# Performance work log

Hardware: AMD Instinct MI355X
Metric: run time of the kernel (lower is better)

## Reference

```python
import jax, jax.numpy as jnp
import numpy as np

B, T, D, H = 512, 128, 384, 6
DH = D // H  # 64
DFF = 4 * D  # 1536
EPS = 1e-5


def layer_norm(x, g, b):
    mu = jnp.mean(x, axis=-1, keepdims=True)
    var = jnp.var(x, axis=-1, keepdims=True)
    return (x - mu) * jax.lax.rsqrt(var + EPS) * g + b


def setup_inputs() -> dict:
    key = jax.random.key(0)
    ks = jax.random.split(key, 12)
    s = lambda *sh: 1.0 / np.sqrt(sh[0])
    return {
        "x": jax.random.normal(ks[0], (B, T, D), dtype=jnp.float32),
        "Wq": jax.random.normal(ks[1], (D, D), dtype=jnp.float32) * s(D),
        "Wk": jax.random.normal(ks[2], (D, D), dtype=jnp.float32) * s(D),
        "Wv": jax.random.normal(ks[3], (D, D), dtype=jnp.float32) * s(D),
        "Wo": jax.random.normal(ks[4], (D, D), dtype=jnp.float32) * s(D),
        "bo": jnp.zeros((D,), jnp.float32),
        "W1": jax.random.normal(ks[5], (D, DFF), dtype=jnp.float32) * s(D),
        "b1": jnp.zeros((DFF,), jnp.float32),
        "W2": jax.random.normal(ks[6], (DFF, D), dtype=jnp.float32) * s(DFF),
        "b2": jnp.zeros((D,), jnp.float32),
        "g1": jnp.ones((D,), jnp.float32),
        "be1": jnp.zeros((D,), jnp.float32),
        "g2": jnp.ones((D,), jnp.float32),
        "be2": jnp.zeros((D,), jnp.float32),
    }


def reference(x, Wq, Wk, Wv, Wo, bo, W1, b1, W2, b2, g1, be1, g2, be2):
    # --- multi-head causal self-attention on layer_norm1(x) ---
    h = layer_norm(x, g1, be1)
    q = (h @ Wq).reshape(B, T, H, DH)
    k = (h @ Wk).reshape(B, T, H, DH)
    v = (h @ Wv).reshape(B, T, H, DH)
    scores = jnp.einsum("bthd,bshd->bhts", q, k) * (DH ** -0.5)  # [B,H,T,T]
    causal = jnp.tril(jnp.ones((T, T), dtype=bool))
    scores = jnp.where(causal, scores, -jnp.inf)
    attn = jax.nn.softmax(scores, axis=-1)
    o = jnp.einsum("bhts,bshd->bthd", attn, v).reshape(B, T, D)
    x = x + o @ Wo + bo
    # --- feed-forward on layer_norm2(x) ---
    h2 = layer_norm(x, g2, be2)
    ff = jax.nn.relu(h2 @ W1 + b1) @ W2 + b2
    return x + ff
```

## Files before the change

### kernel.cpp

```cpp
#include <hip/hip_runtime.h>

#define B_   512
#define T_   128
#define D_   384
#define H_   6
#define DH_  64
#define DFF_ 1536
#define NROW (B_*T_)

typedef __attribute__((ext_vector_type(8))) short bf16x8;
typedef __attribute__((ext_vector_type(4))) float f32x4;

__device__ __forceinline__ unsigned short f2bf(float f) {
  union { float f; unsigned u; } v; v.f = f;
  unsigned r = v.u + 0x7fffu + ((v.u >> 16) & 1u);
  return (unsigned short)(r >> 16);
}

#define GLDS16(gp, lp)                                                     \
  __builtin_amdgcn_global_load_lds(                                        \
      (const __attribute__((address_space(1))) void*)(gp),                 \
      (__attribute__((address_space(3))) void*)(lp), 16, 0, 0)

#define BAR_LGKM() asm volatile("s_waitcnt lgkmcnt(0)\n\ts_barrier" ::: "memory")

__global__ void wt_kernel(const float* __restrict__ W, unsigned short* __restrict__ WT,
                          int K, int Nn) {
  int id = blockIdx.x * 256 + threadIdx.x;
  if (id >= K * Nn) return;
  int n = id % Nn, kk = id / Nn;
  WT[(size_t)n * K + kk] = f2bf(W[(size_t)kk * Nn + n]);
}

__global__ void pack_w1(const unsigned short* __restrict__ W1T,
                        unsigned short* __restrict__ W1P) {
  int tid = blockIdx.x * 256 + threadIdx.x;
  int lane = tid & 63, frag = tid >> 6;
  int k = frag % 12, t2 = frag / 12;
  int mi = t2 & 1, t3 = t2 >> 1;
  int w = t3 & 3, c = t3 >> 2;
  int l15 = lane & 15, lq = lane >> 4;
  int r = c * 128 + w * 32 + mi * 16 + l15;
  int col = k * 32 + lq * 8;
  *(int4*)(W1P + (size_t)tid * 8) = *(const int4*)(W1T + (size_t)r * 384 + col);
}
__global__ void pack_w2(const unsigned short* __restrict__ W2T,
                        unsigned short* __restrict__ W2P) {
  int tid = blockIdx.x * 256 + threadIdx.x;
  int lane = tid & 63, frag = tid >> 6;
  int kk = frag & 3, t2 = frag >> 2;
  int c = t2 % 12, t3 = t2 / 12;
  int mi = t3 % 6, w = t3 / 6;
  int l15 = lane & 15, lq = lane >> 4;
  int r = w * 96 + mi * 16 + l15;
  int col = c * 128 + kk * 32 + lq * 8;
  *(int4*)(W2P + (size_t)tid * 8) = *(const int4*)(W2T + (size_t)r * 1536 + col);
}

__global__ __launch_bounds__(256) void ln_kernel(const float* __restrict__ x,
                                                 const float* __restrict__ g,
                                                 const float* __restrict__ be,
                                                 unsigned short* __restrict__ out) {
  int row = (blockIdx.x * 256 + threadIdx.x) >> 6;
  int l = threadIdx.x & 63;
  const float* xr = x + (size_t)row * D_;
  float v[6]; float s = 0.f, ss = 0.f;
  #pragma unroll
  for (int i = 0; i < 6; ++i) { v[i] = xr[l + i*64]; s += v[i]; ss += v[i]*v[i]; }
  #pragma unroll
  for (int m = 1; m < 64; m <<= 1) { s += __shfl_xor(s, m); ss += __shfl_xor(ss, m); }
  float mu  = s * (1.f / D_);
  float var = ss * (1.f / D_) - mu * mu;
  float rs  = rsqrtf(var + 1e-5f);
  unsigned short* orow = out + (size_t)row * D_;
  #pragma unroll
  for (int i = 0; i < 6; ++i) {
    int c = l + i*64;
    orow[c] = f2bf((v[i] - mu) * rs * g[c] + be[c]);
  }
}

template<int EPI>
__global__ __launch_bounds__(256) void gemm_bt(const unsigned short* __restrict__ A,
                                               const unsigned short* __restrict__ BT,
                                               void* __restrict__ Cc,
                                               const float* __restrict__ bias,
                                               const float* __restrict__ res,
                                               int Nn, int K) {
  __shared__ unsigned short As[2][128][32];
  __shared__ unsigned short Bs[2][128][32];
  int tid = threadIdx.x, w = tid >> 6, l = tid & 63;
  int wr = w >> 1, wc = w & 1;
  size_t R0 = (size_t)blockIdx.x * 128;
  int C0 = blockIdx.y * 128;

  int seg0 = (w * 2 + 0) * 16;
  int seg1 = (w * 2 + 1) * 16;
  int srow0 = seg0 + (l >> 2);
  int srow1 = seg1 + (l >> 2);
  int scol  = (l & 3) * 8;

  const unsigned short* ga0 = A  + (R0 + srow0) * K + scol;
  const unsigned short* ga1 = A  + (R0 + srow1) * K + scol;
  const unsigned short* gb0 = BT + (size_t)(C0 + srow0) * K + scol;
  const unsigned short* gb1 = BT + (size_t)(C0 + srow1) * K + scol;

  f32x4 acc[4][4];
  #pragma unroll
  for (int i = 0; i < 4; ++i)
    #pragma unroll
    for (int j = 0; j < 4; ++j) acc[i][j] = (f32x4){0.f, 0.f, 0.f, 0.f};

  GLDS16(ga0, &As[0][seg0][0]);
  GLDS16(ga1, &As[0][seg1][0]);
  GLDS16(gb0, &Bs[0][seg0][0]);
  GLDS16(gb1, &Bs[0][seg1][0]);
  ga0 += 32; ga1 += 32; gb0 += 32; gb1 += 32;

  int nk = K >> 5;
  for (int t = 0; t < nk; ++t) {
    int cur = t & 1;
    __syncthreads();
    if (t + 1 < nk) {
      GLDS16(ga0, &As[cur ^ 1][seg0][0]);
      GLDS16(ga1, &As[cur ^ 1][seg1][0]);
      GLDS16(gb0, &Bs[cur ^ 1][seg0][0]);
      GLDS16(gb1, &Bs[cur ^ 1][seg1][0]);
      ga0 += 32; ga1 += 32; gb0 += 32; gb1 += 32;
    }
    bf16x8 af[4], bf[4];
    #pragma unroll
    for (int mi = 0; mi < 4; ++mi)
      af[mi] = *(const bf16x8*)(&As[cur][wr*64 + mi*16 + (l & 15)][(l >> 4) * 8]);
    #pragma unroll
    for (int ni = 0; ni < 4; ++ni)
      bf[ni] = *(const bf16x8*)(&Bs[cur][wc*64 + ni*16 + (l & 15)][(l >> 4) * 8]);
    #pragma unroll
    for (int mi = 0; mi < 4; ++mi)
      #pragma unroll
      for (int ni = 0; ni < 4; ++ni)
        acc[mi][ni] = __builtin_amdgcn_mfma_f32_16x16x32_bf16(af[mi], bf[ni], acc[mi][ni], 0, 0, 0);
  }

  #pragma unroll
  for (int mi = 0; mi < 4; ++mi) {
    #pragma unroll
    for (int ni = 0; ni < 4; ++ni) {
      int col = C0 + wc*64 + ni*16 + (l & 15);
      #pragma unroll
      for (int j = 0; j < 4; ++j) {
        size_t row = R0 + wr*64 + mi*16 + ((l >> 4) << 2) + j;
        float vv = acc[mi][ni][j];
        if (EPI == 1) {
          ((float*)Cc)[row * Nn + col] = vv + bias[col] + res[row * Nn + col];
        } else {
          int buf = col / 384, c2 = col - buf * 384;
          ((unsigned short*)Cc)[(size_t)buf * NROW * 384 + row * 384 + c2] = f2bf(vv);
        }
      }
    }
  }
}

#define LDA3(dst, pA, k0)                                                    \
  { _Pragma("unroll") for (int kq = 0; kq < 3; ++kq)                         \
      dst[kq] = *(const bf16x8*)((pA) + ((k0) + kq) * 512); }

#define CMP3(buf, k0, acc)                                                   \
  { _Pragma("unroll") for (int kq = 0; kq < 3; ++kq) {                       \
      bf16x8 bfr[4];                                                         \
      _Pragma("unroll") for (int ni = 0; ni < 4; ++ni)                       \
        bfr[ni] = *(const bf16x8*)(smem + (ni*12 + (k0)+kq)*1024 + l*16);    \
      _Pragma("unroll") for (int ni = 0; ni < 4; ++ni)                       \
        acc[ni] = __builtin_amdgcn_mfma_f32_16x16x32_bf16(                   \
            buf[kq], bfr[ni], acc[ni], 0, 0, 0);                             \
    } }

__global__ __launch_bounds__(512, 4) void ffn_fused(
    const unsigned short* __restrict__ h2,
    const unsigned short* __restrict__ w1P,
    const unsigned short* __restrict__ w2P,
    const float* __restrict__ b1,
    const float* __restrict__ b2,
    float* __restrict__ out)
{
  __shared__ __align__(16) char smem[65536];
  int tid = threadIdx.x, w = tid >> 6, l = tid & 63;
  int l15 = l & 15, lq = l >> 4;
  size_t R0 = (size_t)blockIdx.x * 64;

  {
    int row = tid >> 3, gi = row >> 4, l15w = row & 15;
    int cbase = (tid & 7) * 48;
    const unsigned short* src = h2 + (R0 + row) * 384 + cbase;
    #pragma unroll
    for (int i = 0; i < 6; ++i) {
      int col = cbase + i * 8;
      int k = col >> 5, lqw = (col >> 3) & 3;
      *(int4*)(smem + (gi*12 + k)*1024 + (lqw*16 + l15w)*16) = *(const int4*)(src + i*8);
    }
  }
  __syncthreads();

  f32x4 oacc[3][4];
  #pragma unroll
  for (int i = 0; i < 3; ++i)
    #pragma unroll
    for (int j = 0; j < 4; ++j) oacc[i][j] = (f32x4){0.f, 0.f, 0.f, 0.f};

  const unsigned short* w1b = w1P + w * 6144  + l * 8;
  const unsigned short* w2b = w2P + w * 73728 + l * 8;

  #define LDV(dst, pV, kk)                                                   \
    { _Pragma("unroll") for (int mi = 0; mi < 3; ++mi)                       \
        dst[mi] = *(const bf16x8*)((pV) + mi * 24576 + (kk) * 512); }

  #define CMPV(buf, kk)                                                      \
    { bf16x8 bv[4];                                                          \
      _Pragma("unroll") for (int ni = 0; ni < 4; ++ni)                       \
        bv[ni] = *(const bf16x8*)(smem + 49152 + (ni*4 + (kk))*1024 + l*16); \
      _Pragma("unroll") for (int mi = 0; mi < 3; ++mi)                       \
        _Pragma("unroll") for (int ni = 0; ni < 4; ++ni)                     \
          oacc[mi][ni] = __builtin_amdgcn_mfma_f32_16x16x32_bf16(            \
              buf[mi], bv[ni], oacc[mi][ni], 0, 0, 0);                       \
    }

  bf16x8 afA[3], afB[3];
  bf16x8 avA[3], avB[3];

  LDA3(afA, w1b, 0)

  for (int c = 0; c < 12; ++c) {
    const unsigned short* pA = w1b + (size_t)c * 49152;
    const unsigned short* pV = w2b + c * 2048;

    f32x4 pacc[4];
    #pragma unroll
    for (int j = 0; j < 4; ++j) pacc[j] = (f32x4){0.f, 0.f, 0.f, 0.f};

    LDA3(afB, pA, 3)
    __builtin_amdgcn_s_setprio(1); CMP3(afA, 0, pacc) __builtin_amdgcn_s_setprio(0);
    LDA3(afA, pA, 6)
    __builtin_amdgcn_s_setprio(1); CMP3(afB, 3, pacc) __builtin_amdgcn_s_setprio(0);
    LDA3(afB, pA, 9)
    __builtin_amdgcn_s_setprio(1); CMP3(afA, 6, pacc) __builtin_amdgcn_s_setprio(0);
    LDV(avA, pV, 0)
    __builtin_amdgcn_s_setprio(1); CMP3(afB, 9, pacc) __builtin_amdgcn_s_setprio(0);

    {
      int fcb = c * 128 + w * 16 + lq * 4;
      float4 bb = *(const float4*)(b1 + fcb);
      unsigned pw = (unsigned)(49152 + (w >> 1) * 1024 +
                    (((w & 1) * 2 + (lq >> 1)) * 16 + l15) * 16 + (lq & 1) * 8);
      #pragma unroll
      for (int ni = 0; ni < 4; ++ni) {
        float p0 = pacc[ni][0] + bb.x;
        float p1 = pacc[ni][1] + bb.y;
        float p2 = pacc[ni][2] + bb.z;
        float p3 = pacc[ni][3] + bb.w;
        ushort4 pk;
        pk.x = f2bf(p0 > 0.f ? p0 : 0.f);
        pk.y = f2bf(p1 > 0.f ? p1 : 0.f);
        pk.z = f2bf(p2 > 0.f ? p2 : 0.f);
        pk.w = f2bf(p3 > 0.f ? p3 : 0.f);
        *(ushort4*)(smem + pw + ni * 4096) = pk;
      }
    }
    BAR_LGKM();

    const unsigned short* pAn = w1b + (size_t)(c < 11 ? c + 1 : 11) * 49152;
    LDV(avB, pV, 1)
    __builtin_amdgcn_s_setprio(1); CMPV(avA, 0) __builtin_amdgcn_s_setprio(0);
    LDV(avA, pV, 2)
    __builtin_amdgcn_s_setprio(1); CMPV(avB, 1) __builtin_amdgcn_s_setprio(0);
    LDV(avB, pV, 3)
    __builtin_amdgcn_s_setprio(1); CMPV(avA, 2) __builtin_amdgcn_s_setprio(0);
    LDA3(afA, pAn, 0)
    __builtin_amdgcn_s_setprio(1); CMPV(avB, 3) __builtin_amdgcn_s_setprio(0);
    BAR_LGKM();
  }
  #undef LDV
  #undef CMPV

  #pragma unroll
  for (int mi = 0; mi < 3; ++mi) {
    int ocb = w * 48 + mi * 16 + lq * 4;
    float4 b2v = *(const float4*)(b2 + ocb);
    #pragma unroll
    for (int ni = 0; ni < 4; ++ni) {
      size_t row = R0 + ni * 16 + l15;
      float* op = out + row * D_ + ocb;
      float4 r = *(const float4*)op;
      float4 o;
      o.x = oacc[mi][ni][0] + b2v.x + r.x;
      o.y = oacc[mi][ni][1] + b2v.y + r.y;
      o.z = oacc[mi][ni][2] + b2v.z + r.z;
      o.w = oacc[mi][ni][3] + b2v.w + r.w;
      *(float4*)op = o;
    }
  }
}

__global__ __launch_bounds__(256) void attn_kernel(const unsigned short* __restrict__ q,
                                                   const unsigned short* __restrict__ k,
                                                   const unsigned short* __restrict__ v,
                                                   unsigned short* __restrict__ o) {
  __shared__ __align__(16) char smem[52224];
  unsigned short (*Ks)[72]       = (unsigned short(*)[72])smem;
  unsigned short (*Ps)[32][136]  = (unsigned short(*)[32][136])smem;
  unsigned short (*Vt)[136]      = (unsigned short(*)[136])(smem + 34816);

  int bh = blockIdx.x;
  int b = bh / H_, h = bh % H_;
  int tid = threadIdx.x, w = tid >> 6, l = tid & 63;

  const unsigned short* kb = k + ((size_t)b * T_) * D_ + h * DH_;
  const unsigned short* vb = v + ((size_t)b * T_) * D_ + h * DH_;
  #pragma unroll
  for (int it = 0; it < 4; ++it) {
    int id = it * 256 + tid;
    int s = id >> 3, c8 = (id & 7) * 8;
    int4 kv = *(const int4*)(kb + (size_t)s * D_ + c8);
    *(int4*)(&Ks[s][c8]) = kv;
    int4 vv = *(const int4*)(vb + (size_t)s * D_ + c8);
    const unsigned short* pe = (const unsigned short*)&vv;
    #pragma unroll
    for (int j2 = 0; j2 < 8; ++j2) Vt[c8 + j2][s] = pe[j2];
  }
  __syncthreads();

  const unsigned short* qbp = q + ((size_t)b * T_) * D_ + h * DH_;
  int rowbase = w * 32;
  bf16x8 aq[2][2];
  #pragma unroll
  for (int mi = 0; mi < 2; ++mi)
    #pragma unroll
    for (int ks = 0; ks < 2; ++ks)
      aq[mi][ks] = *(const bf16x8*)(qbp + (size_t)(rowbase + mi*16 + (l & 15)) * D_
                                        + ks*32 + ((l >> 4) << 3));

  f32x4 accs[2][8];
  #pragma unroll
  for (int i = 0; i < 2; ++i)
    #pragma unroll
    for (int j = 0; j < 8; ++j) accs[i][j] = (f32x4){0.f, 0.f, 0.f, 0.f};
  #pragma unroll
  for (int ks = 0; ks < 2; ++ks) {
    bf16x8 bk[8];
    #pragma unroll
    for (int ni = 0; ni < 8; ++ni)
      bk[ni] = *(const bf16x8*)(&Ks[ni*16 + (l & 15)][ks*32 + ((l >> 4) << 3)]);
    __builtin_amdgcn_s_setprio(1);
    #pragma unroll
    for (int mi = 0; mi < 2; ++mi)
      #pragma unroll
      for (int ni = 0; ni < 8; ++ni)
        accs[mi][ni] = __builtin_amdgcn_mfma_f32_16x16x32_bf16(aq[mi][ks], bk[ni], accs[mi][ni], 0, 0, 0);
    __builtin_amdgcn_s_setprio(0);
  }
  __syncthreads();

  #pragma unroll
  for (int mi = 0; mi < 2; ++mi) {
    #pragma unroll
    for (int j = 0; j < 4; ++j) {
      int t = rowbase + mi*16 + ((l >> 4) << 2) + j;
      float mx = -1e30f;
      #pragma unroll
      for (int ni = 0; ni < 8; ++ni) {
        int scol = ni*16 + (l & 15);
        float sv = accs[mi][ni][j] * 0.125f;
        sv = (scol <= t) ? sv : -1e30f;
        accs[mi][ni][j] = sv;
        mx = fmaxf(mx, sv);
      }
      mx = fmaxf(mx, __shfl_xor(mx, 1));
      mx = fmaxf(mx, __shfl_xor(mx, 2));
      mx = fmaxf(mx, __shfl_xor(mx, 4));
      mx = fmaxf(mx, __shfl_xor(mx, 8));
      float sum = 0.f;
      #pragma unroll
      for (int ni = 0; ni < 8; ++ni) {
        float e = __expf(accs[mi][ni][j] - mx);
        accs[mi][ni][j] = e;
        sum += e;
      }
      sum += __shfl_xor(sum, 1);
      sum += __shfl_xor(sum, 2);
      sum += __shfl_xor(sum, 4);
      sum += __shfl_xor(sum, 8);
      float inv = 1.f / sum;
      #pragma unroll
      for (int ni = 0; ni < 8; ++ni)
        Ps[w][mi*16 + ((l >> 4) << 2) + j][ni*16 + (l & 15)] = f2bf(accs[mi][ni][j] * inv);
    }
  }
  __syncthreads();

  f32x4 acco[2][4];
  #pragma unroll
  for (int i = 0; i < 2; ++i)
    #pragma unroll
    for (int j = 0; j < 4; ++j) acco[i][j] = (f32x4){0.f, 0.f, 0.f, 0.f};
  #pragma unroll
  for (int ks = 0; ks < 4; ++ks) {
    bf16x8 ap[2], bv[4];
    #pragma unroll
    for (int mi = 0; mi < 2; ++mi)
      ap[mi] = *(const bf16x8*)(&Ps[w][mi*16 + (l & 15)][ks*32 + ((l >> 4) << 3)]);
    #pragma unroll
    for (int ni = 0; ni < 4; ++ni)
      bv[ni] = *(const bf16x8*)(&Vt[ni*16 + (l & 15)][ks*32 + ((l >> 4) << 3)]);
    __builtin_amdgcn_s_setprio(1);
    #pragma unroll
    for (int mi = 0; mi < 2; ++mi)
      #pragma unroll
      for (int ni = 0; ni < 4; ++ni)
        acco[mi][ni] = __builtin_amdgcn_mfma_f32_16x16x32_bf16(ap[mi], bv[ni], acco[mi][ni], 0, 0, 0);
    __builtin_amdgcn_s_setprio(0);
  }

  unsigned short* ob = o + ((size_t)b * T_) * D_ + h * DH_;
  #pragma unroll
  for (int mi = 0; mi < 2; ++mi)
    #pragma unroll
    for (int ni = 0; ni < 4; ++ni)
      #pragma unroll
      for (int j = 0; j < 4; ++j) {
        int t = rowbase + mi*16 + ((l >> 4) << 2) + j;
        int d = ni*16 + (l & 15);
        ob[(size_t)t * D_ + d] = f2bf(acco[mi][ni][j]);
      }
}

extern "C" void kernel_launch(void* const* d_in, const int* in_sizes, int n_in,
                              void* d_out, int out_size, void* d_ws, size_t ws_size,
                              hipStream_t stream) {
  const float* x   = (const float*)d_in[0];
  const float* Wq  = (const float*)d_in[1];
  const float* Wk  = (const float*)d_in[2];
  const float* Wv  = (const float*)d_in[3];
  const float* Wo  = (const float*)d_in[4];
  const float* bo  = (const float*)d_in[5];
  const float* W1  = (const float*)d_in[6];
  const float* b1  = (const float*)d_in[7];
  const float* W2  = (const float*)d_in[8];
  const float* b2  = (const float*)d_in[9];
  const float* g1  = (const float*)d_in[10];
  const float* be1 = (const float*)d_in[11];
  const float* g2  = (const float*)d_in[12];
  const float* be2 = (const float*)d_in[13];

  char* ws = (char*)d_ws;
  unsigned short* hb   = (unsigned short*)(ws);
  unsigned short* qb   = (unsigned short*)(ws +  50331648);
  unsigned short* kbuf = (unsigned short*)(ws + 100663296);
  unsigned short* vbuf = (unsigned short*)(ws + 150994944);
  unsigned short* wqT  = (unsigned short*)(ws + 201326592);
  unsigned short* wkT  = wqT + 147456;
  unsigned short* wvT  = wkT + 147456;
  unsigned short* woT  = wvT + 147456;
  unsigned short* w1T  = woT + 147456;
  unsigned short* w2T  = w1T + 589824;
  unsigned short* w1P  = w2T + 589824;
  unsigned short* w2P  = w1P + 589824;
  float* x2 = (float*)d_out;
  (void)kbuf; (void)vbuf;

  wt_kernel<<<dim3(576),  256, 0, stream>>>(Wq, wqT, 384, 384);
  wt_kernel<<<dim3(576),  256, 0, stream>>>(Wk, wkT, 384, 384);
  wt_kernel<<<dim3(576),  256, 0, stream>>>(Wv, wvT, 384, 384);
  wt_kernel<<<dim3(576),  256, 0, stream>>>(Wo, woT, 384, 384);
  wt_kernel<<<dim3(2304), 256, 0, stream>>>(W1, w1T, 384, 1536);
  wt_kernel<<<dim3(2304), 256, 0, stream>>>(W2, w2T, 1536, 384);
  pack_w1<<<dim3(288), 256, 0, stream>>>(w1T, w1P);
  pack_w2<<<dim3(288), 256, 0, stream>>>(w2T, w2P);

  ln_kernel<<<dim3(NROW / 4), 256, 0, stream>>>(x, g1, be1, hb);

  gemm_bt<3><<<dim3(NROW / 128, 9), 256, 0, stream>>>(hb, wqT, qb, nullptr, nullptr, 1152, 384);

  attn_kernel<<<dim3(B_ * H_), 256, 0, stream>>>(qb, kbuf, vbuf, qb);

  gemm_bt<1><<<dim3(NROW / 128, 3), 256, 0, stream>>>(qb, woT, x2, bo, x, 384, 384);

  ln_kernel<<<dim3(NROW / 4), 256, 0, stream>>>((const float*)x2, g2, be2, hb);

  ffn_fused<<<dim3(NROW / 64), 512, 0, stream>>>(hb, w1P, w2P, b1, b2, x2);
}
```

Measured before the change: 453.3 us.

## Use 32x32x16 MFMA for FFN first GEMM with 256-wide hidden chunks

Restructures the fused FFN kernel so the W1 GEMM uses 32x32x16 bf16 MFMA instructions over 256-column hidden chunks (6 iterations instead of 12), with a new W1 packing layout and h2 LDS layout to match. The second GEMM consumes 8 k-steps per chunk, which halves the number of barriers per row block. The intent is to cut LDS fragment reads and loop overhead per FLOP. In exchange the kernel needs 80KB of dynamic shared memory, which can reduce occupancy, and it drops the register double-buffered prefetch of weights used before.

```diff
diff --git a/kernel.cpp b/kernel.cpp
--- a/kernel.cpp
+++ b/kernel.cpp
@@ -10,6 +10,7 @@
 
 typedef __attribute__((ext_vector_type(8))) short bf16x8;
 typedef __attribute__((ext_vector_type(4))) float f32x4;
+typedef __attribute__((ext_vector_type(16))) float f32x16;
 
 __device__ __forceinline__ unsigned short f2bf(float f) {
   union { float f; unsigned u; } v; v.f = f;
@@ -32,17 +33,15 @@
   WT[(size_t)n * K + kk] = f2bf(W[(size_t)kk * Nn + n]);
 }
 
-__global__ void pack_w1(const unsigned short* __restrict__ W1T,
-                        unsigned short* __restrict__ W1P) {
+__global__ void pack_w1_32(const unsigned short* __restrict__ W1T,
+                           unsigned short* __restrict__ W1P) {
   int tid = blockIdx.x * 256 + threadIdx.x;
   int lane = tid & 63, frag = tid >> 6;
-  int k = frag % 12, t2 = frag / 12;
-  int mi = t2 & 1, t3 = t2 >> 1;
-  int w = t3 & 3, c = t3 >> 2;
-  int l15 = lane & 15, lq = lane >> 4;
-  int r = c * 128 + w * 32 + mi * 16 + l15;
-  int col = k * 32 + lq * 8;
-  *(int4*)(W1P + (size_t)tid * 8) = *(const int4*)(W1T + (size_t)r * 384 + col);
+  int k16 = frag % 24, t = frag / 24;
+  int w = t & 7, c6 = t >> 3;
+  int row = c6 * 256 + w * 32 + (lane & 31);
+  int col = k16 * 16 + (lane >> 5) * 8;
+  *(int4*)(W1P + (size_t)tid * 8) = *(const int4*)(W1T + (size_t)row * 384 + col);
 }
 __global__ void pack_w2(const unsigned short* __restrict__ W2T,
                         unsigned short* __restrict__ W2P) {
@@ -162,20 +161,6 @@
   }
 }
 
-#define LDA3(dst, pA, k0)                                                    \
-  { _Pragma("unroll") for (int kq = 0; kq < 3; ++kq)                         \
-      dst[kq] = *(const bf16x8*)((pA) + ((k0) + kq) * 512); }
-
-#define CMP3(buf, k0, acc)                                                   \
-  { _Pragma("unroll") for (int kq = 0; kq < 3; ++kq) {                       \
-      bf16x8 bfr[4];                                                         \
-      _Pragma("unroll") for (int ni = 0; ni < 4; ++ni)                       \
-        bfr[ni] = *(const bf16x8*)(smem + (ni*12 + (k0)+kq)*1024 + l*16);    \
-      _Pragma("unroll") for (int ni = 0; ni < 4; ++ni)                       \
-        acc[ni] = __builtin_amdgcn_mfma_f32_16x16x32_bf16(                   \
-            buf[kq], bfr[ni], acc[ni], 0, 0, 0);                             \
-    } }
-
 __global__ __launch_bounds__(512, 4) void ffn_fused(
     const unsigned short* __restrict__ h2,
     const unsigned short* __restrict__ w1P,
@@ -184,20 +169,20 @@
     const float* __restrict__ b2,
     float* __restrict__ out)
 {
-  __shared__ __align__(16) char smem[65536];
+  extern __shared__ __align__(16) char smem[];
   int tid = threadIdx.x, w = tid >> 6, l = tid & 63;
   int l15 = l & 15, lq = l >> 4;
   size_t R0 = (size_t)blockIdx.x * 64;
 
   {
-    int row = tid >> 3, gi = row >> 4, l15w = row & 15;
-    int cbase = (tid & 7) * 48;
-    const unsigned short* src = h2 + (R0 + row) * 384 + cbase;
+    int row = tid >> 3, nt = row >> 5, r31 = row & 31;
+    const unsigned short* src = h2 + (R0 + row) * 384;
     #pragma unroll
     for (int i = 0; i < 6; ++i) {
-      int col = cbase + i * 8;
-      int k = col >> 5, lqw = (col >> 3) & 3;
-      *(int4*)(smem + (gi*12 + k)*1024 + (lqw*16 + l15w)*16) = *(const int4*)(src + i*8);
+      int c8 = (tid & 7) + i * 8;
+      int k16 = c8 >> 1, hi = c8 & 1;
+      *(int4*)(smem + (nt*24 + k16)*1024 + (hi*32 + r31)*16) =
+          *(const int4*)(src + c8 * 8);
     }
   }
   __syncthreads();
@@ -208,79 +193,79 @@
     #pragma unroll
     for (int j = 0; j < 4; ++j) oacc[i][j] = (f32x4){0.f, 0.f, 0.f, 0.f};
 
-  const unsigned short* w1b = w1P + w * 6144  + l * 8;
+  const unsigned short* w1b = w1P + w * 12288 + l * 8;
   const unsigned short* w2b = w2P + w * 73728 + l * 8;
 
-  #define LDV(dst, pV, kk)                                                   \
-    { _Pragma("unroll") for (int mi = 0; mi < 3; ++mi)                       \
-        dst[mi] = *(const bf16x8*)((pV) + mi * 24576 + (kk) * 512); }
-
-  #define CMPV(buf, kk)                                                      \
-    { bf16x8 bv[4];                                                          \
-      _Pragma("unroll") for (int ni = 0; ni < 4; ++ni)                       \
-        bv[ni] = *(const bf16x8*)(smem + 49152 + (ni*4 + (kk))*1024 + l*16); \
-      _Pragma("unroll") for (int mi = 0; mi < 3; ++mi)                       \
-        _Pragma("unroll") for (int ni = 0; ni < 4; ++ni)                     \
-          oacc[mi][ni] = __builtin_amdgcn_mfma_f32_16x16x32_bf16(            \
-              buf[mi], bv[ni], oacc[mi][ni], 0, 0, 0);                       \
-    }
-
-  bf16x8 afA[3], afB[3];
-  bf16x8 avA[3], avB[3];
-
-  LDA3(afA, w1b, 0)
-
-  for (int c = 0; c < 12; ++c) {
-    const unsigned short* pA = w1b + (size_t)c * 49152;
-    const unsigned short* pV = w2b + c * 2048;
-
-    f32x4 pacc[4];
-    #pragma unroll
-    for (int j = 0; j < 4; ++j) pacc[j] = (f32x4){0.f, 0.f, 0.f, 0.f};
-
-    LDA3(afB, pA, 3)
-    __builtin_amdgcn_s_setprio(1); CMP3(afA, 0, pacc) __builtin_amdgcn_s_setprio(0);
-    LDA3(afA, pA, 6)
-    __builtin_amdgcn_s_setprio(1); CMP3(afB, 3, pacc) __builtin_amdgcn_s_setprio(0);
-    LDA3(afB, pA, 9)
-    __builtin_amdgcn_s_setprio(1); CMP3(afA, 6, pacc) __builtin_amdgcn_s_setprio(0);
-    LDV(avA, pV, 0)
-    __builtin_amdgcn_s_setprio(1); CMP3(afB, 9, pacc) __builtin_amdgcn_s_setprio(0);
+  for (int c = 0; c < 6; ++c) {
+    const unsigned short* pA = w1b + (size_t)c * 98304;
+    const unsigned short* pV = w2b + c * 4096;
+
+    f32x16 pacc[2];
+    pacc[0] = (f32x16)(0.f);
+    pacc[1] = (f32x16)(0.f);
+
+    #pragma unroll
+    for (int g = 0; g < 6; ++g) {
+      bf16x8 af[4];
+      #pragma unroll
+      for (int kq = 0; kq < 4; ++kq)
+        af[kq] = *(const bf16x8*)(pA + (g*4 + kq) * 512);
+      __builtin_amdgcn_s_setprio(1);
+      #pragma unroll
+      for (int kq = 0; kq < 4; ++kq) {
+        bf16x8 b0 = *(const bf16x8*)(smem + ((g*4 + kq))*1024 + l*16);
+        bf16x8 b1f = *(const bf16x8*)(smem + (24 + g*4 + kq)*1024 + l*16);
+        pacc[0] = __builtin_amdgcn_mfma_f32_32x32x16_bf16(af[kq], b0,  pacc[0], 0, 0, 0);
+        pacc[1] = __builtin_amdgcn_mfma_f32_32x32x16_bf16(af[kq], b1f, pacc[1], 0, 0, 0);
+      }
+      __builtin_amdgcn_s_setprio(0);
+    }
 
     {
-      int fcb = c * 128 + w * 16 + lq * 4;
-      float4 bb = *(const float4*)(b1 + fcb);
-      unsigned pw = (unsigned)(49152 + (w >> 1) * 1024 +
-                    (((w & 1) * 2 + (lq >> 1)) * 16 + l15) * 16 + (lq & 1) * 8);
-      #pragma unroll
-      for (int ni = 0; ni < 4; ++ni) {
-        float p0 = pacc[ni][0] + bb.x;
-        float p1 = pacc[ni][1] + bb.y;
-        float p2 = pacc[ni][2] + bb.z;
-        float p3 = pacc[ni][3] + bb.w;
-        ushort4 pk;
-        pk.x = f2bf(p0 > 0.f ? p0 : 0.f);
-        pk.y = f2bf(p1 > 0.f ? p1 : 0.f);
-        pk.z = f2bf(p2 > 0.f ? p2 : 0.f);
-        pk.w = f2bf(p3 > 0.f ? p3 : 0.f);
-        *(ushort4*)(smem + pw + ni * 4096) = pk;
+      int hi = l >> 5, r31 = l & 31;
+      int niB = r31 >> 4;
+      #pragma unroll
+      for (int nt = 0; nt < 2; ++nt) {
+        int ni = nt*2 + niB;
+        #pragma unroll
+        for (int q = 0; q < 4; ++q) {
+          int fcb = c * 256 + w * 32 + q * 8 + hi * 4;
+          float4 bb = *(const float4*)(b1 + fcb);
+          float p0 = ((nt == 0) ? pacc[0][q*4+0] : pacc[1][q*4+0]) + bb.x;
+          float p1 = ((nt == 0) ? pacc[0][q*4+1] : pacc[1][q*4+1]) + bb.y;
+          float p2 = ((nt == 0) ? pacc[0][q*4+2] : pacc[1][q*4+2]) + bb.z;
+          float p3 = ((nt == 0) ? pacc[0][q*4+3] : pacc[1][q*4+3]) + bb.w;
+          ushort4 pk;
+          pk.x = f2bf(p0 > 0.f ? p0 : 0.f);
+          pk.y = f2bf(p1 > 0.f ? p1 : 0.f);
+          pk.z = f2bf(p2 > 0.f ? p2 : 0.f);
+          pk.w = f2bf(p3 > 0.f ? p3 : 0.f);
+          *(ushort4*)(smem + 49152 + (ni*8 + w)*1024 + (q*16 + l15)*16 + hi*8) = pk;
+        }
       }
     }
     BAR_LGKM();
 
-    const unsigned short* pAn = w1b + (size_t)(c < 11 ? c + 1 : 11) * 49152;
-    LDV(avB, pV, 1)
-    __builtin_amdgcn_s_setprio(1); CMPV(avA, 0) __builtin_amdgcn_s_setprio(0);
-    LDV(avA, pV, 2)
-    __builtin_amdgcn_s_setprio(1); CMPV(avB, 1) __builtin_amdgcn_s_setprio(0);
-    LDV(avB, pV, 3)
-    __builtin_amdgcn_s_setprio(1); CMPV(avA, 2) __builtin_amdgcn_s_setprio(0);
-    LDA3(afA, pAn, 0)
-    __builtin_amdgcn_s_setprio(1); CMPV(avB, 3) __builtin_amdgcn_s_setprio(0);
+    #pragma unroll
+    for (int kk = 0; kk < 8; ++kk) {
+      bf16x8 av[3];
+      #pragma unroll
+      for (int mi = 0; mi < 3; ++mi)
+        av[mi] = *(const bf16x8*)(pV + mi*24576 + (kk>>2)*2048 + (kk&3)*512);
+      bf16x8 bv[4];
+      #pragma unroll
+      for (int ni = 0; ni < 4; ++ni)
+        bv[ni] = *(const bf16x8*)(smem + 49152 + (ni*8 + kk)*1024 + l*16);
+      __builtin_amdgcn_s_setprio(1);
+      #pragma unroll
+      for (int mi = 0; mi < 3; ++mi)
+        #pragma unroll
+        for (int ni = 0; ni < 4; ++ni)
+          oacc[mi][ni] = __builtin_amdgcn_mfma_f32_16x16x32_bf16(av[mi], bv[ni], oacc[mi][ni], 0, 0, 0);
+      __builtin_amdgcn_s_setprio(0);
+    }
     BAR_LGKM();
   }
-  #undef LDV
-  #undef CMPV
 
   #pragma unroll
   for (int mi = 0; mi < 3; ++mi) {
@@ -467,13 +452,20 @@
   float* x2 = (float*)d_out;
   (void)kbuf; (void)vbuf;
 
+  static bool attr_set = false;
+  if (!attr_set) {
+    hipFuncSetAttribute(reinterpret_cast<const void*>(ffn_fused),
+                        hipFuncAttributeMaxDynamicSharedMemorySize, 81920);
+    attr_set = true;
+  }
+
   wt_kernel<<<dim3(576),  256, 0, stream>>>(Wq, wqT, 384, 384);
   wt_kernel<<<dim3(576),  256, 0, stream>>>(Wk, wkT, 384, 384);
   wt_kernel<<<dim3(576),  256, 0, stream>>>(Wv, wvT, 384, 384);
   wt_kernel<<<dim3(576),  256, 0, stream>>>(Wo, woT, 384, 384);
   wt_kernel<<<dim3(2304), 256, 0, stream>>>(W1, w1T, 384, 1536);
   wt_kernel<<<dim3(2304), 256, 0, stream>>>(W2, w2T, 1536, 384);
-  pack_w1<<<dim3(288), 256, 0, stream>>>(w1T, w1P);
+  pack_w1_32<<<dim3(288), 256, 0, stream>>>(w1T, w1P);
   pack_w2<<<dim3(288), 256, 0, stream>>>(w2T, w2P);
 
   ln_kernel<<<dim3(NROW / 4), 256, 0, stream>>>(x, g1, be1, hb);
@@ -486,5 +478,5 @@
 
   ln_kernel<<<dim3(NROW / 4), 256, 0, stream>>>((const float*)x2, g2, be2, hb);
 
-  ffn_fused<<<dim3(NROW / 64), 512, 0, stream>>>(hb, w1P, w2P, b1, b2, x2);
-}
+  ffn_fused<<<dim3(NROW / 64), 512, 81920, stream>>>(hb, w1P, w2P, b1, b2, x2);
+}
```

New measurement: 459.3 us. Within noise of the previous version (+1.3%).
